# Kernel optimization log

Hardware: AMD Instinct MI355X
Metric: run time of the kernel (lower is better)

Reference implementation:

```python
import jax, jax.numpy as jnp
import numpy as np

B, S, I, H, O, E, K = 2, 2048, 4096, 1376, 4096, 8, 2
BALANCE_W = 0.01  # balance_loss_weight in llama-moe


def setup_inputs() -> dict:
    key = jax.random.key(0)
    ks = jax.random.split(key, 6)
    sc = lambda k, shape, fan: jax.random.normal(k, shape, jnp.float32) * (fan ** -0.5)
    return {
        "x": jax.random.normal(ks[0], (B, S, I), jnp.float32),
        "gate_w": sc(ks[1], (E, I), I),          # linear gate network, no bias
        "w_gate": sc(ks[2], (E, H, I), I),       # GLU gate proj per expert
        "b_gate": jnp.zeros((E, H), jnp.float32),
        "w_up": sc(ks[3], (E, H, I), I),         # GLU up proj per expert
        "b_up": jnp.zeros((E, H), jnp.float32),
        "w_down": sc(ks[4], (E, O, H), H),       # down proj per expert
        "b_down": jnp.zeros((E, O), jnp.float32),
    }


def _cv_squared(v, eps=1e-10):
    # torch: x.var() / (x.mean()**2 + eps), unbiased variance
    mean = jnp.mean(v)
    var = jnp.sum((v - mean) ** 2) / (v.shape[0] - 1)
    return var / (mean ** 2 + eps)


def reference(x, gate_w, w_gate, b_gate, w_up, b_up, w_down, b_down):
    bsz, seq, _ = x.shape
    xt = x.reshape(-1, I)                         # [T, I] tokens
    T = xt.shape[0]

    # ---- TopKBalancedNoisyGate (no-noise branch) ----
    logits = xt @ gate_w.T                        # [T, E]
    top_logits, top_idx = jax.lax.top_k(logits, K)
    top_scores = jax.nn.softmax(top_logits, axis=-1)   # softmax over top-k logits
    # dense routing matrix: zeros.scatter(1, top_idx, top_scores)
    dense = jnp.zeros((T, E), xt.dtype).at[jnp.arange(T)[:, None], top_idx].set(top_scores)
    importance = dense.sum(axis=0)                # [E]
    load = (dense > 0).astype(jnp.float32).sum(axis=0)  # [E]
    gate_loss = BALANCE_W * (_cv_squared(importance) + _cv_squared(load))

    # ---- UniversalCalculator over LinearGLUExperts ----
    # Dense-dispatch formulation: compute every expert on every token, weight by
    # the (mostly-zero) routing matrix -> identical math to gather/grouped-GEMM/scatter.
    g = jnp.einsum('ti,ehi->teh', xt, w_gate) + b_gate        # [T, E, H]
    u = jnp.einsum('ti,ehi->teh', xt, w_up) + b_up            # [T, E, H]
    inter = jax.nn.silu(g) * u                                # GLU
    # score * (W_down h + b_down) == W_down (score*h) + score*b_down
    y = jnp.einsum('teh,eoh->to', inter * dense[:, :, None], w_down) + dense @ b_down
    return y.reshape(bsz, seq, O), gate_loss
```

## Files before the change

kernel.cpp:

```cpp
#include <hip/hip_runtime.h>
#include <hip/hip_bf16.h>
#include <stdint.h>

#define TN 4096
#define DI 4096
#define DH 1376
#define DHP 1408
#define DO 4096
#define NE 8
#define NPAIR 8192

typedef unsigned short u16;
typedef __bf16 bf16x8 __attribute__((ext_vector_type(8)));
typedef float f32x4 __attribute__((ext_vector_type(4)));
typedef uint32_t u32x4 __attribute__((ext_vector_type(4)));

__device__ __forceinline__ uint32_t pack2bf(float a, float b) {
    union { float f; uint32_t u; } ua, ub;
    ua.f = a; ub.f = b;
    uint32_t lo = (ua.u + 0x7fffu + ((ua.u >> 16) & 1u)) >> 16;
    uint32_t hi = (ub.u + 0x7fffu + ((ub.u >> 16) & 1u)) >> 16;
    return lo | (hi << 16);
}
__device__ __forceinline__ u16 f2bf(float a) {
    union { float f; uint32_t u; } ua; ua.f = a;
    return (u16)((ua.u + 0x7fffu + ((ua.u >> 16) & 1u)) >> 16);
}
__device__ __forceinline__ void gload16(const void* g, void* l) {
    __builtin_amdgcn_global_load_lds(
        (const __attribute__((address_space(1))) void*)g,
        (__attribute__((address_space(3))) void*)l, 16, 0, 0);
}

__global__ __launch_bounds__(256) void k_cvt(const float* __restrict__ src,
                                             u16* __restrict__ dst, int n8)
{
    int i = blockIdx.x * 256 + threadIdx.x;
    if (i >= n8) return;
    const float4* s = (const float4*)(src + (size_t)i * 8);
    float4 a = s[0], b = s[1];
    u32x4 q = {pack2bf(a.x, a.y), pack2bf(a.z, a.w), pack2bf(b.x, b.y), pack2bf(b.z, b.w)};
    *(u32x4*)(dst + (size_t)i * 8) = q;
}

__global__ __launch_bounds__(256) void k_cvt_wd(const float* __restrict__ src,
                                                u16* __restrict__ dst)
{
    int i = blockIdx.x * 256 + threadIdx.x;
    int row = i / 176, c8 = (i % 176) * 8;
    u32x4 q = {0u, 0u, 0u, 0u};
    if (c8 < DH) {
        const float4* s = (const float4*)(src + (size_t)row * DH + c8);
        float4 a = s[0], b = s[1];
        q = (u32x4){pack2bf(a.x, a.y), pack2bf(a.z, a.w), pack2bf(b.x, b.y), pack2bf(b.z, b.w)};
    }
    *(u32x4*)(dst + (size_t)row * DHP + c8) = q;
}

__global__ __launch_bounds__(256) void k_gate(
    const float* __restrict__ x, const float* __restrict__ gw,
    u16* __restrict__ x16, int* __restrict__ tke, float* __restrict__ tks,
    int* __restrict__ cnt, float* __restrict__ imp)
{
    int t = blockIdx.x, tid = threadIdx.x;
    const float* xr = x + (size_t)t * DI;
    double acc[NE];
#pragma unroll
    for (int e = 0; e < NE; ++e) acc[e] = 0.0;
#pragma unroll
    for (int j = 0; j < 4; ++j) {
        int i4 = (j * 256 + tid) * 4;
        float4 xv = *(const float4*)(xr + i4);
        uint2 p; p.x = pack2bf(xv.x, xv.y); p.y = pack2bf(xv.z, xv.w);
        *(uint2*)(x16 + (size_t)t * DI + i4) = p;
#pragma unroll
        for (int e = 0; e < NE; ++e) {
            float4 wv = *(const float4*)(gw + (size_t)e * DI + i4);
            acc[e] = fma((double)xv.x, (double)wv.x, acc[e]);
            acc[e] = fma((double)xv.y, (double)wv.y, acc[e]);
            acc[e] = fma((double)xv.z, (double)wv.z, acc[e]);
            acc[e] = fma((double)xv.w, (double)wv.w, acc[e]);
        }
    }
#pragma unroll
    for (int o = 32; o > 0; o >>= 1)
#pragma unroll
        for (int e = 0; e < NE; ++e) acc[e] += __shfl_down(acc[e], o, 64);
    __shared__ double lred[4][NE];
    if ((tid & 63) == 0)
#pragma unroll
        for (int e = 0; e < NE; ++e) lred[tid >> 6][e] = acc[e];
    __syncthreads();
    if (tid == 0) {
        double lg[NE];
#pragma unroll
        for (int e = 0; e < NE; ++e) lg[e] = lred[0][e] + lred[1][e] + lred[2][e] + lred[3][e];
        int e1 = 0;
        for (int e = 1; e < NE; ++e) if (lg[e] > lg[e1]) e1 = e;
        int e2 = -1;
        for (int e = 0; e < NE; ++e) { if (e == e1) continue; if (e2 < 0 || lg[e] > lg[e2]) e2 = e; }
        float d = (float)(lg[e2] - lg[e1]);
        float ed = expf(d);
        float s1 = 1.0f / (1.0f + ed);
        float s2 = ed / (1.0f + ed);
        tke[2 * t] = e1; tke[2 * t + 1] = e2;
        tks[2 * t] = s1; tks[2 * t + 1] = s2;
        atomicAdd(&cnt[e1], 1); atomicAdd(&cnt[e2], 1);
        unsafeAtomicAdd(&imp[e1], s1); unsafeAtomicAdd(&imp[e2], s2);
    }
}

__global__ void k_finalize(const int* __restrict__ cnt, const float* __restrict__ imp,
                           int* __restrict__ off, float* __restrict__ loss_out)
{
    if (threadIdx.x == 0 && blockIdx.x == 0) {
        int o = 0;
        for (int e = 0; e < NE; ++e) { off[e] = o; o += cnt[e]; }
        float m1 = 0.f, m2 = 0.f;
        for (int e = 0; e < NE; ++e) { m1 += imp[e]; m2 += (float)cnt[e]; }
        m1 *= 0.125f; m2 *= 0.125f;
        float v1 = 0.f, v2 = 0.f;
        for (int e = 0; e < NE; ++e) {
            float d1 = imp[e] - m1, d2 = (float)cnt[e] - m2;
            v1 += d1 * d1; v2 += d2 * d2;
        }
        v1 /= 7.0f; v2 /= 7.0f;
        float cv1 = v1 / (m1 * m1 + 1e-10f);
        float cv2 = v2 / (m2 * m2 + 1e-10f);
        *loss_out = 0.01f * (cv1 + cv2);
    }
}

__global__ __launch_bounds__(256) void k_scatter(
    const int* __restrict__ tke, const float* __restrict__ tks,
    const int* __restrict__ off, int* __restrict__ fill,
    int* __restrict__ tok, float* __restrict__ sc)
{
    int t = blockIdx.x * 256 + threadIdx.x;
    if (t >= TN) return;
#pragma unroll
    for (int k = 0; k < 2; ++k) {
        int e = tke[2 * t + k];
        int pos = off[e] + atomicAdd(&fill[e], 1);
        tok[pos] = t; sc[pos] = tks[2 * t + k];
    }
}

__global__ __launch_bounds__(256) void k_yinit(
    const int* __restrict__ tke, const float* __restrict__ tks,
    const float* __restrict__ bd, float* __restrict__ y)
{
    int t = blockIdx.x, tid = threadIdx.x;
    int e1 = tke[2 * t], e2 = tke[2 * t + 1];
    float s1 = tks[2 * t], s2 = tks[2 * t + 1];
    const float4* b1 = (const float4*)(bd + (size_t)e1 * DO);
    const float4* b2 = (const float4*)(bd + (size_t)e2 * DO);
    float4* yr = (float4*)(y + (size_t)t * DO);
#pragma unroll
    for (int j = 0; j < 4; ++j) {
        int i = j * 256 + tid;
        float4 a = b1[i], b = b2[i], r;
        r.x = s1 * a.x + s2 * b.x; r.y = s1 * a.y + s2 * b.y;
        r.z = s1 * a.z + s2 * b.z; r.w = s1 * a.w + s2 * b.w;
        yr[i] = r;
    }
}


__global__ __launch_bounds__(256, 2) void k_stage1f(
    const u16* __restrict__ x16,
    const u16* __restrict__ wg16, const u16* __restrict__ wu16,
    const float* __restrict__ bg, const float* __restrict__ bu,
    const int* __restrict__ cnt, const int* __restrict__ off,
    const int* __restrict__ tok, const float* __restrict__ sc,
    u16* __restrict__ inter)
{
    int e = blockIdx.x & 7;
    int ce = cnt[e];
    int rows0 = (blockIdx.x >> 3) * 128;
    if (rows0 >= ce) return;
    int oe = off[e];
    int h0 = blockIdx.y * 128;
    int tid = threadIdx.x;

    __shared__ u16 As0[128 * 32]; __shared__ u16 As1[128 * 32];
    __shared__ u16 Gs0[128 * 32]; __shared__ u16 Gs1[128 * 32];
    __shared__ u16 Us0[128 * 32]; __shared__ u16 Us1[128 * 32];

    int swz = ((tid & 3) ^ ((tid >> 3) & 3)) * 8;
    const u16* ab0; const u16* ab1; const u16* gb0; const u16* gb1;
    const u16* ub0; const u16* ub1;
    {
        int rl0 = tid >> 2, rl1 = 64 + (tid >> 2);
        int rg0 = oe + min(rows0 + rl0, ce - 1);
        int rg1 = oe + min(rows0 + rl1, ce - 1);
        ab0 = x16 + (size_t)tok[rg0] * DI + swz;
        ab1 = x16 + (size_t)tok[rg1] * DI + swz;
        int hr0 = min(h0 + rl0, DH - 1), hr1 = min(h0 + rl1, DH - 1);
        gb0 = wg16 + ((size_t)e * DH + hr0) * DI + swz;
        gb1 = wg16 + ((size_t)e * DH + hr1) * DI + swz;
        ub0 = wu16 + ((size_t)e * DH + hr0) * DI + swz;
        ub1 = wu16 + ((size_t)e * DH + hr1) * DI + swz;
    }

    int wid = tid >> 6, lane = tid & 63;
    int ldsw = wid * 512;
    int wm = wid >> 1, wn = wid & 1;
    int rA = wm * 64 + (lane & 15);
    int rB = wn * 64 + (lane & 15);
    int colb = (((lane >> 4) ^ ((lane >> 1) & 3)) & 3) * 8;

    f32x4 accg[4][4], accu[4][4];
    f32x4 vz = {0.f, 0.f, 0.f, 0.f};
#pragma unroll
    for (int m = 0; m < 4; ++m)
#pragma unroll
        for (int n = 0; n < 4; ++n) { accg[m][n] = vz; accu[m][n] = vz; }

#define S1_STAGE(A_, G_, U_, K0)                                   \
    do {                                                           \
        gload16(ab0 + (K0), &A_[ldsw]);                            \
        gload16(ab1 + (K0), &A_[2048 + ldsw]);                     \
        gload16(gb0 + (K0), &G_[ldsw]);                            \
        gload16(gb1 + (K0), &G_[2048 + ldsw]);                     \
        gload16(ub0 + (K0), &U_[ldsw]);                            \
        gload16(ub1 + (K0), &U_[2048 + ldsw]);                     \
    } while (0)

#define S1_COMPUTE(A_, G_, U_)                                     \
    do {                                                           \
        bf16x8 a[4], g[4], u[4];                                   \
        _Pragma("unroll")                                          \
        for (int m = 0; m < 4; ++m)                                \
            a[m] = *(const bf16x8*)&A_[(rA + m * 16) * 32 + colb]; \
        _Pragma("unroll")                                          \
        for (int n = 0; n < 4; ++n) {                              \
            g[n] = *(const bf16x8*)&G_[(rB + n * 16) * 32 + colb]; \
            u[n] = *(const bf16x8*)&U_[(rB + n * 16) * 32 + colb]; \
        }                                                          \
        _Pragma("unroll")                                          \
        for (int m = 0; m < 4; ++m)                                \
            _Pragma("unroll")                                      \
            for (int n = 0; n < 4; ++n) {                          \
                accg[m][n] = __builtin_amdgcn_mfma_f32_16x16x32_bf16(a[m], g[n], accg[m][n], 0, 0, 0); \
                accu[m][n] = __builtin_amdgcn_mfma_f32_16x16x32_bf16(a[m], u[n], accu[m][n], 0, 0, 0); \
            }                                                      \
    } while (0)

    S1_STAGE(As0, Gs0, Us0, 0);
    __syncthreads();

    const int NT = DI / 32;
    for (int kt = 0; kt < NT; kt += 2) {
        if (kt + 1 < NT) S1_STAGE(As1, Gs1, Us1, (kt + 1) * 32);
        S1_COMPUTE(As0, Gs0, Us0);
        __syncthreads();
        if (kt + 2 < NT) S1_STAGE(As0, Gs0, Us0, (kt + 2) * 32);
        S1_COMPUTE(As1, Gs1, Us1);
        __syncthreads();
    }
#undef S1_STAGE
#undef S1_COMPUTE

    int rmax = ce - rows0;
    float bgv[4], buv[4];
    int hc[4]; bool hok[4];
#pragma unroll
    for (int n = 0; n < 4; ++n) {
        hc[n] = h0 + wn * 64 + n * 16 + (lane & 15);
        hok[n] = hc[n] < DH;
        bgv[n] = hok[n] ? bg[e * DH + hc[n]] : 0.f;
        buv[n] = hok[n] ? bu[e * DH + hc[n]] : 0.f;
    }
#pragma unroll
    for (int m = 0; m < 4; ++m) {
#pragma unroll
        for (int r = 0; r < 4; ++r) {
            int rl = wm * 64 + m * 16 + (lane >> 4) * 4 + r;
            if (rl < rmax) {
                int rg = oe + rows0 + rl;
                float s = sc[rg];
                size_t rowb = (size_t)rg * DHP;
#pragma unroll
                for (int n = 0; n < 4; ++n) {
                    float v = 0.f;
                    if (hok[n]) {
                        float gv = accg[m][n][r] + bgv[n];
                        float uv = accu[m][n][r] + buv[n];
                        float sig = 1.0f / (1.0f + __expf(-gv));
                        v = s * gv * sig * uv;
                    }
                    inter[rowb + hc[n]] = f2bf(v);
                }
            }
        }
    }
}

__global__ __launch_bounds__(256, 2) void k_stage2f(
    const u16* __restrict__ inter, const u16* __restrict__ wd16,
    const int* __restrict__ cnt, const int* __restrict__ off,
    const int* __restrict__ tok, float* __restrict__ y)
{
    int e = blockIdx.x & 7;
    int ce = cnt[e];
    int rows0 = (blockIdx.x >> 3) * 128;
    if (rows0 >= ce) return;
    int oe = off[e];
    int o0 = blockIdx.y * 128;
    int tid = threadIdx.x;

    __shared__ u16 As0[128 * 32]; __shared__ u16 As1[128 * 32];
    __shared__ u16 Bs0[128 * 32]; __shared__ u16 Bs1[128 * 32];

    int swz = ((tid & 3) ^ ((tid >> 3) & 3)) * 8;
    const u16* ab0; const u16* ab1; const u16* bb0; const u16* bb1;
    {
        int rl0 = tid >> 2, rl1 = 64 + (tid >> 2);
        int ar0 = min(oe + rows0 + rl0, NPAIR - 1);
        int ar1 = min(oe + rows0 + rl1, NPAIR - 1);
        ab0 = inter + (size_t)ar0 * DHP + swz;
        ab1 = inter + (size_t)ar1 * DHP + swz;
        bb0 = wd16 + ((size_t)e * DO + (o0 + rl0)) * DHP + swz;
        bb1 = wd16 + ((size_t)e * DO + (o0 + rl1)) * DHP + swz;
    }

    int wid = tid >> 6, lane = tid & 63;
    int ldsw = wid * 512;
    int wm = wid >> 1, wn = wid & 1;
    int rA = wm * 64 + (lane & 15);
    int rB = wn * 64 + (lane & 15);
    int colb = (((lane >> 4) ^ ((lane >> 1) & 3)) & 3) * 8;

    f32x4 acc[4][4];
    f32x4 vz = {0.f, 0.f, 0.f, 0.f};
#pragma unroll
    for (int m = 0; m < 4; ++m)
#pragma unroll
        for (int n = 0; n < 4; ++n) acc[m][n] = vz;

#define S2_STAGE(A_, B_, K0)                                       \
    do {                                                           \
        gload16(ab0 + (K0), &A_[ldsw]);                            \
        gload16(ab1 + (K0), &A_[2048 + ldsw]);                     \
        gload16(bb0 + (K0), &B_[ldsw]);                            \
        gload16(bb1 + (K0), &B_[2048 + ldsw]);                     \
    } while (0)

#define S2_COMPUTE(A_, B_)                                         \
    do {                                                           \
        bf16x8 a[4], b[4];                                         \
        _Pragma("unroll")                                          \
        for (int m = 0; m < 4; ++m)                                \
            a[m] = *(const bf16x8*)&A_[(rA + m * 16) * 32 + colb]; \
        _Pragma("unroll")                                          \
        for (int n = 0; n < 4; ++n)                                \
            b[n] = *(const bf16x8*)&B_[(rB + n * 16) * 32 + colb]; \
        _Pragma("unroll")                                          \
        for (int m = 0; m < 4; ++m)                                \
            _Pragma("unroll")                                      \
            for (int n = 0; n < 4; ++n)                            \
                acc[m][n] = __builtin_amdgcn_mfma_f32_16x16x32_bf16(a[m], b[n], acc[m][n], 0, 0, 0); \
    } while (0)

    S2_STAGE(As0, Bs0, 0);
    __syncthreads();

    const int NT = DHP / 32;
    for (int kt = 0; kt < NT; kt += 2) {
        if (kt + 1 < NT) S2_STAGE(As1, Bs1, (kt + 1) * 32);
        S2_COMPUTE(As0, Bs0);
        __syncthreads();
        if (kt + 2 < NT) S2_STAGE(As0, Bs0, (kt + 2) * 32);
        S2_COMPUTE(As1, Bs1);
        __syncthreads();
    }
#undef S2_STAGE
#undef S2_COMPUTE

    int rmax = ce - rows0;
#pragma unroll
    for (int m = 0; m < 4; ++m) {
#pragma unroll
        for (int r = 0; r < 4; ++r) {
            int rl = wm * 64 + m * 16 + (lane >> 4) * 4 + r;
            if (rl >= rmax) continue;
            int t = tok[oe + rows0 + rl];
            float* yr = y + (size_t)t * DO + o0 + wn * 64 + (lane & 15);
#pragma unroll
            for (int n = 0; n < 4; ++n)
                unsafeAtomicAdd(yr + n * 16, acc[m][n][r]);
        }
    }
}

extern "C" void kernel_launch(void* const* d_in, const int* in_sizes, int n_in,
                              void* d_out, int out_size, void* d_ws, size_t ws_size,
                              hipStream_t stream)
{
    const float* x  = (const float*)d_in[0];
    const float* gw = (const float*)d_in[1];
    const float* wg = (const float*)d_in[2];
    const float* bg = (const float*)d_in[3];
    const float* wu = (const float*)d_in[4];
    const float* bu = (const float*)d_in[5];
    const float* wd = (const float*)d_in[6];
    const float* bd = (const float*)d_in[7];
    float* y = (float*)d_out;
    float* loss = y + (size_t)TN * DO;

    uint8_t* ws = (uint8_t*)d_ws;
    u16*   x16   = (u16*)(ws + 0);
    u16*   inter = (u16*)(ws + 33554432ull);
    u16*   wg16  = (u16*)(ws + 56623104ull);
    u16*   wu16  = (u16*)(ws + 146800640ull);
    u16*   wd16  = (u16*)(ws + 236978176ull);
    int*   tok   = (int*)(ws + 329252864ull);
    float* sc    = (float*)(ws + 329285632ull);
    int*   tke   = (int*)(ws + 329318400ull);
    float* tks   = (float*)(ws + 329351168ull);
    int*   misc  = (int*)(ws + 329383936ull);
    int* cnt = misc; int* fill = misc + 8; int* off = misc + 16;
    float* imp = (float*)(misc + 24);

    hipMemsetAsync(misc, 0, 128, stream);
    k_cvt<<<22016, 256, 0, stream>>>(wg, wg16, 5636096);
    k_cvt<<<22016, 256, 0, stream>>>(wu, wu16, 5636096);
    k_cvt_wd<<<22528, 256, 0, stream>>>(wd, wd16);
    k_gate<<<TN, 256, 0, stream>>>(x, gw, x16, tke, tks, cnt, imp);
    k_finalize<<<1, 64, 0, stream>>>(cnt, imp, off, loss);
    k_scatter<<<TN / 256, 256, 0, stream>>>(tke, tks, off, fill, tok, sc);
    k_yinit<<<TN, 256, 0, stream>>>(tke, tks, bd, y);
    k_stage1f<<<dim3(256, 11), 256, 0, stream>>>(x16, wg16, wu16, bg, bu, cnt, off, tok, sc, inter);
    k_stage2f<<<dim3(256, 32), 256, 0, stream>>>(inter, wd16, cnt, off, tok, y);
}
```

Measured before the change: 801.2 us.

## Triple-buffer LDS pipeline with vmcnt waits and MFMA priority in expert GEMMs

Both grouped expert GEMM kernels move from a double-buffered loop with __syncthreads to a three-stage LDS ring. Two tiles of global->LDS loads stay in flight, and each stage waits only on its own loads through explicit s_waitcnt vmcnt counts plus raw s_barrier. Wave priority is raised around the MFMA block so compute issues ahead of the loads. This is meant to hide global load latency better, at the cost of 50% more LDS per block, which may limit occupancy. The hand-counted vmcnt values make correctness depend on the exact number of loads per stage.

```diff
diff --git a/kernel.cpp b/kernel.cpp
--- a/kernel.cpp
+++ b/kernel.cpp
@@ -31,6 +31,7 @@
         (const __attribute__((address_space(1))) void*)g,
         (__attribute__((address_space(3))) void*)l, 16, 0, 0);
 }
+#define MEMFENCE() asm volatile("" ::: "memory")
 
 __global__ __launch_bounds__(256) void k_cvt(const float* __restrict__ src,
                                              u16* __restrict__ dst, int n8)
@@ -167,7 +168,7 @@
 }
 
 
-__global__ __launch_bounds__(256, 2) void k_stage1f(
+__global__ __launch_bounds__(256, 2) void k_stage1g(
     const u16* __restrict__ x16,
     const u16* __restrict__ wg16, const u16* __restrict__ wu16,
     const float* __restrict__ bg, const float* __restrict__ bu,
@@ -183,9 +184,9 @@
     int h0 = blockIdx.y * 128;
     int tid = threadIdx.x;
 
-    __shared__ u16 As0[128 * 32]; __shared__ u16 As1[128 * 32];
-    __shared__ u16 Gs0[128 * 32]; __shared__ u16 Gs1[128 * 32];
-    __shared__ u16 Us0[128 * 32]; __shared__ u16 Us1[128 * 32];
+    __shared__ u16 As0[128 * 32]; __shared__ u16 As1[128 * 32]; __shared__ u16 As2[128 * 32];
+    __shared__ u16 Gs0[128 * 32]; __shared__ u16 Gs1[128 * 32]; __shared__ u16 Gs2[128 * 32];
+    __shared__ u16 Us0[128 * 32]; __shared__ u16 Us1[128 * 32]; __shared__ u16 Us2[128 * 32];
 
     int swz = ((tid & 3) ^ ((tid >> 3) & 3)) * 8;
     const u16* ab0; const u16* ab1; const u16* gb0; const u16* gb1;
@@ -238,6 +239,7 @@
             g[n] = *(const bf16x8*)&G_[(rB + n * 16) * 32 + colb]; \
             u[n] = *(const bf16x8*)&U_[(rB + n * 16) * 32 + colb]; \
         }                                                          \
+        __builtin_amdgcn_s_setprio(1);                             \
         _Pragma("unroll")                                          \
         for (int m = 0; m < 4; ++m)                                \
             _Pragma("unroll")                                      \
@@ -245,22 +247,43 @@
                 accg[m][n] = __builtin_amdgcn_mfma_f32_16x16x32_bf16(a[m], g[n], accg[m][n], 0, 0, 0); \
                 accu[m][n] = __builtin_amdgcn_mfma_f32_16x16x32_bf16(a[m], u[n], accu[m][n], 0, 0, 0); \
             }                                                      \
-    } while (0)
-
+        __builtin_amdgcn_s_setprio(0);                             \
+    } while (0)
+
+#define S1_PHASE(A_, G_, U_, KN)                                   \
+    do {                                                           \
+        asm volatile("s_waitcnt vmcnt(12)" ::: "memory");          \
+        __builtin_amdgcn_s_barrier();                              \
+        MEMFENCE();                                                \
+        S1_COMPUTE(A_, G_, U_);                                    \
+        __builtin_amdgcn_s_barrier();                              \
+        MEMFENCE();                                                \
+        S1_STAGE(A_, G_, U_, KN);                                  \
+    } while (0)
+
+    const int NT = DI / 32;
+    const int KL = (NT - 1) * 32;
     S1_STAGE(As0, Gs0, Us0, 0);
-    __syncthreads();
-
-    const int NT = DI / 32;
-    for (int kt = 0; kt < NT; kt += 2) {
-        if (kt + 1 < NT) S1_STAGE(As1, Gs1, Us1, (kt + 1) * 32);
-        S1_COMPUTE(As0, Gs0, Us0);
-        __syncthreads();
-        if (kt + 2 < NT) S1_STAGE(As0, Gs0, Us0, (kt + 2) * 32);
-        S1_COMPUTE(As1, Gs1, Us1);
-        __syncthreads();
-    }
+    S1_STAGE(As1, Gs1, Us1, 32);
+    S1_STAGE(As2, Gs2, Us2, 64);
+
+    for (int kt = 0; kt + 4 < NT; kt += 3) {
+        S1_PHASE(As0, Gs0, Us0, min((kt + 3) * 32, KL));
+        S1_PHASE(As1, Gs1, Us1, min((kt + 4) * 32, KL));
+        S1_PHASE(As2, Gs2, Us2, min((kt + 5) * 32, KL));
+    }
+    asm volatile("s_waitcnt vmcnt(12)" ::: "memory");
+    __builtin_amdgcn_s_barrier();
+    MEMFENCE();
+    S1_COMPUTE(As0, Gs0, Us0);
+    asm volatile("s_waitcnt vmcnt(6)" ::: "memory");
+    __builtin_amdgcn_s_barrier();
+    MEMFENCE();
+    S1_COMPUTE(As1, Gs1, Us1);
+    asm volatile("s_waitcnt vmcnt(0)" ::: "memory");
 #undef S1_STAGE
 #undef S1_COMPUTE
+#undef S1_PHASE
 
     int rmax = ce - rows0;
     float bgv[4], buv[4];
@@ -297,7 +320,7 @@
     }
 }
 
-__global__ __launch_bounds__(256, 2) void k_stage2f(
+__global__ __launch_bounds__(256, 2) void k_stage2g(
     const u16* __restrict__ inter, const u16* __restrict__ wd16,
     const int* __restrict__ cnt, const int* __restrict__ off,
     const int* __restrict__ tok, float* __restrict__ y)
@@ -310,8 +333,8 @@
     int o0 = blockIdx.y * 128;
     int tid = threadIdx.x;
 
-    __shared__ u16 As0[128 * 32]; __shared__ u16 As1[128 * 32];
-    __shared__ u16 Bs0[128 * 32]; __shared__ u16 Bs1[128 * 32];
+    __shared__ u16 As0[128 * 32]; __shared__ u16 As1[128 * 32]; __shared__ u16 As2[128 * 32];
+    __shared__ u16 Bs0[128 * 32]; __shared__ u16 Bs1[128 * 32]; __shared__ u16 Bs2[128 * 32];
 
     int swz = ((tid & 3) ^ ((tid >> 3) & 3)) * 8;
     const u16* ab0; const u16* ab1; const u16* bb0; const u16* bb1;
@@ -356,27 +379,49 @@
         _Pragma("unroll")                                          \
         for (int n = 0; n < 4; ++n)                                \
             b[n] = *(const bf16x8*)&B_[(rB + n * 16) * 32 + colb]; \
+        __builtin_amdgcn_s_setprio(1);                             \
         _Pragma("unroll")                                          \
         for (int m = 0; m < 4; ++m)                                \
             _Pragma("unroll")                                      \
             for (int n = 0; n < 4; ++n)                            \
                 acc[m][n] = __builtin_amdgcn_mfma_f32_16x16x32_bf16(a[m], b[n], acc[m][n], 0, 0, 0); \
-    } while (0)
-
+        __builtin_amdgcn_s_setprio(0);                             \
+    } while (0)
+
+#define S2_PHASE(A_, B_, KN)                                       \
+    do {                                                           \
+        asm volatile("s_waitcnt vmcnt(8)" ::: "memory");           \
+        __builtin_amdgcn_s_barrier();                              \
+        MEMFENCE();                                                \
+        S2_COMPUTE(A_, B_);                                        \
+        __builtin_amdgcn_s_barrier();                              \
+        MEMFENCE();                                                \
+        S2_STAGE(A_, B_, KN);                                      \
+    } while (0)
+
+    const int NT = DHP / 32;
+    const int KL = (NT - 1) * 32;
     S2_STAGE(As0, Bs0, 0);
-    __syncthreads();
-
-    const int NT = DHP / 32;
-    for (int kt = 0; kt < NT; kt += 2) {
-        if (kt + 1 < NT) S2_STAGE(As1, Bs1, (kt + 1) * 32);
-        S2_COMPUTE(As0, Bs0);
-        __syncthreads();
-        if (kt + 2 < NT) S2_STAGE(As0, Bs0, (kt + 2) * 32);
-        S2_COMPUTE(As1, Bs1);
-        __syncthreads();
-    }
+    S2_STAGE(As1, Bs1, 32);
+    S2_STAGE(As2, Bs2, 64);
+
+    for (int kt = 0; kt + 4 < NT; kt += 3) {
+        S2_PHASE(As0, Bs0, min((kt + 3) * 32, KL));
+        S2_PHASE(As1, Bs1, min((kt + 4) * 32, KL));
+        S2_PHASE(As2, Bs2, min((kt + 5) * 32, KL));
+    }
+    asm volatile("s_waitcnt vmcnt(8)" ::: "memory");
+    __builtin_amdgcn_s_barrier();
+    MEMFENCE();
+    S2_COMPUTE(As0, Bs0);
+    asm volatile("s_waitcnt vmcnt(4)" ::: "memory");
+    __builtin_amdgcn_s_barrier();
+    MEMFENCE();
+    S2_COMPUTE(As1, Bs1);
+    asm volatile("s_waitcnt vmcnt(0)" ::: "memory");
 #undef S2_STAGE
 #undef S2_COMPUTE
+#undef S2_PHASE
 
     int rmax = ce - rows0;
 #pragma unroll
@@ -431,6 +476,6 @@
     k_finalize<<<1, 64, 0, stream>>>(cnt, imp, off, loss);
     k_scatter<<<TN / 256, 256, 0, stream>>>(tke, tks, off, fill, tok, sc);
     k_yinit<<<TN, 256, 0, stream>>>(tke, tks, bd, y);
-    k_stage1f<<<dim3(256, 11), 256, 0, stream>>>(x16, wg16, wu16, bg, bu, cnt, off, tok, sc, inter);
-    k_stage2f<<<dim3(256, 32), 256, 0, stream>>>(inter, wd16, cnt, off, tok, y);
-}
+    k_stage1g<<<dim3(256, 11), 256, 0, stream>>>(x16, wg16, wu16, bg, bu, cnt, off, tok, sc, inter);
+    k_stage2g<<<dim3(256, 32), 256, 0, stream>>>(inter, wd16, cnt, off, tok, y);
+}
```

Result: no change. 793.4 us (-1.0%).

## Keep two K-tiles in flight with explicit vmcnt waits and MFMA priority

Applied to the files above, without the earlier changes.

Both grouped-GEMM kernels are restructured so two stages of global-to-LDS loads are always outstanding. Each stage waits only on the older batch with s_waitcnt vmcnt(N) and a raw s_barrier, where before every __syncthreads drained all loads. The MFMA block is wrapped in s_setprio(1)/s_setprio(0) so the matrix math gets issue priority over other waves. The goal is to hide global memory latency behind compute, at the cost of relying on hand-counted vmcnt values that must match the number of loads issued per stage.

```diff
diff --git a/kernel.cpp b/kernel.cpp
--- a/kernel.cpp
+++ b/kernel.cpp
@@ -31,6 +31,7 @@
         (const __attribute__((address_space(1))) void*)g,
         (__attribute__((address_space(3))) void*)l, 16, 0, 0);
 }
+#define MEMFENCE() asm volatile("" ::: "memory")
 
 __global__ __launch_bounds__(256) void k_cvt(const float* __restrict__ src,
                                              u16* __restrict__ dst, int n8)
@@ -167,7 +168,7 @@
 }
 
 
-__global__ __launch_bounds__(256, 2) void k_stage1f(
+__global__ __launch_bounds__(256, 2) void k_stage1h(
     const u16* __restrict__ x16,
     const u16* __restrict__ wg16, const u16* __restrict__ wu16,
     const float* __restrict__ bg, const float* __restrict__ bu,
@@ -238,6 +239,7 @@
             g[n] = *(const bf16x8*)&G_[(rB + n * 16) * 32 + colb]; \
             u[n] = *(const bf16x8*)&U_[(rB + n * 16) * 32 + colb]; \
         }                                                          \
+        __builtin_amdgcn_s_setprio(1);                             \
         _Pragma("unroll")                                          \
         for (int m = 0; m < 4; ++m)                                \
             _Pragma("unroll")                                      \
@@ -245,20 +247,37 @@
                 accg[m][n] = __builtin_amdgcn_mfma_f32_16x16x32_bf16(a[m], g[n], accg[m][n], 0, 0, 0); \
                 accu[m][n] = __builtin_amdgcn_mfma_f32_16x16x32_bf16(a[m], u[n], accu[m][n], 0, 0, 0); \
             }                                                      \
+        __builtin_amdgcn_s_setprio(0);                             \
     } while (0)
 
+    const int NT = DI / 32;
     S1_STAGE(As0, Gs0, Us0, 0);
-    __syncthreads();
-
-    const int NT = DI / 32;
-    for (int kt = 0; kt < NT; kt += 2) {
-        if (kt + 1 < NT) S1_STAGE(As1, Gs1, Us1, (kt + 1) * 32);
+    S1_STAGE(As1, Gs1, Us1, 32);
+
+    for (int kt = 0; kt < NT - 2; kt += 2) {
+        asm volatile("s_waitcnt vmcnt(6)" ::: "memory");
+        __builtin_amdgcn_s_barrier();
+        MEMFENCE();
         S1_COMPUTE(As0, Gs0, Us0);
-        __syncthreads();
-        if (kt + 2 < NT) S1_STAGE(As0, Gs0, Us0, (kt + 2) * 32);
+        __builtin_amdgcn_s_barrier();
+        MEMFENCE();
+        S1_STAGE(As0, Gs0, Us0, (kt + 2) * 32);
+        asm volatile("s_waitcnt vmcnt(6)" ::: "memory");
+        __builtin_amdgcn_s_barrier();
+        MEMFENCE();
         S1_COMPUTE(As1, Gs1, Us1);
-        __syncthreads();
-    }
+        __builtin_amdgcn_s_barrier();
+        MEMFENCE();
+        S1_STAGE(As1, Gs1, Us1, (kt + 3) * 32);
+    }
+    asm volatile("s_waitcnt vmcnt(6)" ::: "memory");
+    __builtin_amdgcn_s_barrier();
+    MEMFENCE();
+    S1_COMPUTE(As0, Gs0, Us0);
+    asm volatile("s_waitcnt vmcnt(0)" ::: "memory");
+    __builtin_amdgcn_s_barrier();
+    MEMFENCE();
+    S1_COMPUTE(As1, Gs1, Us1);
 #undef S1_STAGE
 #undef S1_COMPUTE
 
@@ -297,7 +316,7 @@
     }
 }
 
-__global__ __launch_bounds__(256, 2) void k_stage2f(
+__global__ __launch_bounds__(256, 2) void k_stage2h(
     const u16* __restrict__ inter, const u16* __restrict__ wd16,
     const int* __restrict__ cnt, const int* __restrict__ off,
     const int* __restrict__ tok, float* __restrict__ y)
@@ -356,25 +375,43 @@
         _Pragma("unroll")                                          \
         for (int n = 0; n < 4; ++n)                                \
             b[n] = *(const bf16x8*)&B_[(rB + n * 16) * 32 + colb]; \
+        __builtin_amdgcn_s_setprio(1);                             \
         _Pragma("unroll")                                          \
         for (int m = 0; m < 4; ++m)                                \
             _Pragma("unroll")                                      \
             for (int n = 0; n < 4; ++n)                            \
                 acc[m][n] = __builtin_amdgcn_mfma_f32_16x16x32_bf16(a[m], b[n], acc[m][n], 0, 0, 0); \
+        __builtin_amdgcn_s_setprio(0);                             \
     } while (0)
 
+    const int NT = DHP / 32;
     S2_STAGE(As0, Bs0, 0);
-    __syncthreads();
-
-    const int NT = DHP / 32;
-    for (int kt = 0; kt < NT; kt += 2) {
-        if (kt + 1 < NT) S2_STAGE(As1, Bs1, (kt + 1) * 32);
+    S2_STAGE(As1, Bs1, 32);
+
+    for (int kt = 0; kt < NT - 2; kt += 2) {
+        asm volatile("s_waitcnt vmcnt(4)" ::: "memory");
+        __builtin_amdgcn_s_barrier();
+        MEMFENCE();
         S2_COMPUTE(As0, Bs0);
-        __syncthreads();
-        if (kt + 2 < NT) S2_STAGE(As0, Bs0, (kt + 2) * 32);
+        __builtin_amdgcn_s_barrier();
+        MEMFENCE();
+        S2_STAGE(As0, Bs0, (kt + 2) * 32);
+        asm volatile("s_waitcnt vmcnt(4)" ::: "memory");
+        __builtin_amdgcn_s_barrier();
+        MEMFENCE();
         S2_COMPUTE(As1, Bs1);
-        __syncthreads();
-    }
+        __builtin_amdgcn_s_barrier();
+        MEMFENCE();
+        S2_STAGE(As1, Bs1, (kt + 3) * 32);
+    }
+    asm volatile("s_waitcnt vmcnt(4)" ::: "memory");
+    __builtin_amdgcn_s_barrier();
+    MEMFENCE();
+    S2_COMPUTE(As0, Bs0);
+    asm volatile("s_waitcnt vmcnt(0)" ::: "memory");
+    __builtin_amdgcn_s_barrier();
+    MEMFENCE();
+    S2_COMPUTE(As1, Bs1);
 #undef S2_STAGE
 #undef S2_COMPUTE
 
@@ -431,6 +468,6 @@
     k_finalize<<<1, 64, 0, stream>>>(cnt, imp, off, loss);
     k_scatter<<<TN / 256, 256, 0, stream>>>(tke, tks, off, fill, tok, sc);
     k_yinit<<<TN, 256, 0, stream>>>(tke, tks, bd, y);
-    k_stage1f<<<dim3(256, 11), 256, 0, stream>>>(x16, wg16, wu16, bg, bu, cnt, off, tok, sc, inter);
-    k_stage2f<<<dim3(256, 32), 256, 0, stream>>>(inter, wd16, cnt, off, tok, y);
-}
+    k_stage1h<<<dim3(256, 11), 256, 0, stream>>>(x16, wg16, wu16, bg, bu, cnt, off, tok, sc, inter);
+    k_stage2h<<<dim3(256, 32), 256, 0, stream>>>(inter, wd16, cnt, off, tok, y);
+}
```

After: 800.0 us. No clear change (-0.2%).

## Rewrite grouped GEMM kernels with 512-thread 256-row tiles and ping-pong schedule

Applied to the files above, without the earlier changes.

Both expert GEMM stages move to 512-thread blocks with 256-row token tiles, K-step 64, and an 8-way XOR-swizzled LDS layout. The main loop interleaves LDS reads, async global-to-LDS loads and MFMA bursts between explicit barriers, with s_setprio raised around the MFMA bursts. Stage 2 also widens its output tile to 256 columns, so each wave holds 8x4 accumulators. This is meant to raise data reuse per LDS byte and overlap loads with compute. In exchange it uses more LDS and registers per block, and for small experts more of each 256-row tile is padding.

```diff
diff --git a/kernel.cpp b/kernel.cpp
--- a/kernel.cpp
+++ b/kernel.cpp
@@ -31,6 +31,11 @@
         (const __attribute__((address_space(1))) void*)g,
         (__attribute__((address_space(3))) void*)l, 16, 0, 0);
 }
+#define MEMFENCE() asm volatile("" ::: "memory")
+#define VMCNT0()   asm volatile("s_waitcnt vmcnt(0)" ::: "memory")
+#define BAR()      do { MEMFENCE(); __builtin_amdgcn_s_barrier(); MEMFENCE(); } while (0)
+#define LGKM()     do { asm volatile("s_waitcnt lgkmcnt(0)" ::: "memory"); \
+                        __builtin_amdgcn_sched_barrier(0); } while (0)
 
 __global__ __launch_bounds__(256) void k_cvt(const float* __restrict__ src,
                                              u16* __restrict__ dst, int n8)
@@ -167,7 +172,7 @@
 }
 
 
-__global__ __launch_bounds__(256, 2) void k_stage1f(
+__global__ __launch_bounds__(512, 2) void k_s1_8p(
     const u16* __restrict__ x16,
     const u16* __restrict__ wg16, const u16* __restrict__ wu16,
     const float* __restrict__ bg, const float* __restrict__ bu,
@@ -177,38 +182,38 @@
 {
     int e = blockIdx.x & 7;
     int ce = cnt[e];
-    int rows0 = (blockIdx.x >> 3) * 128;
+    int rows0 = (blockIdx.x >> 3) * 256;
     if (rows0 >= ce) return;
     int oe = off[e];
     int h0 = blockIdx.y * 128;
     int tid = threadIdx.x;
 
-    __shared__ u16 As0[128 * 32]; __shared__ u16 As1[128 * 32];
-    __shared__ u16 Gs0[128 * 32]; __shared__ u16 Gs1[128 * 32];
-    __shared__ u16 Us0[128 * 32]; __shared__ u16 Us1[128 * 32];
-
-    int swz = ((tid & 3) ^ ((tid >> 3) & 3)) * 8;
-    const u16* ab0; const u16* ab1; const u16* gb0; const u16* gb1;
-    const u16* ub0; const u16* ub1;
-    {
-        int rl0 = tid >> 2, rl1 = 64 + (tid >> 2);
-        int rg0 = oe + min(rows0 + rl0, ce - 1);
-        int rg1 = oe + min(rows0 + rl1, ce - 1);
-        ab0 = x16 + (size_t)tok[rg0] * DI + swz;
-        ab1 = x16 + (size_t)tok[rg1] * DI + swz;
-        int hr0 = min(h0 + rl0, DH - 1), hr1 = min(h0 + rl1, DH - 1);
-        gb0 = wg16 + ((size_t)e * DH + hr0) * DI + swz;
-        gb1 = wg16 + ((size_t)e * DH + hr1) * DI + swz;
-        ub0 = wu16 + ((size_t)e * DH + hr0) * DI + swz;
-        ub1 = wu16 + ((size_t)e * DH + hr1) * DI + swz;
+    __shared__ u16 Aa[256 * 64]; __shared__ u16 Ab[256 * 64];
+    __shared__ u16 Ga[128 * 64]; __shared__ u16 Gb[128 * 64];
+    __shared__ u16 Ua[128 * 64]; __shared__ u16 Ub[128 * 64];
+
+    int swz = ((tid & 7) ^ ((tid >> 3) & 7)) * 8;
+    int rr = tid >> 3;
+    const u16* ap[4]; const u16* gp[2]; const u16* up[2];
+#pragma unroll
+    for (int i = 0; i < 4; ++i) {
+        int rg = oe + min(rows0 + i * 64 + rr, ce - 1);
+        ap[i] = x16 + (size_t)tok[rg] * DI + swz;
+    }
+#pragma unroll
+    for (int j = 0; j < 2; ++j) {
+        int hr = min(h0 + j * 64 + rr, DH - 1);
+        gp[j] = wg16 + ((size_t)e * DH + hr) * DI + swz;
+        up[j] = wu16 + ((size_t)e * DH + hr) * DI + swz;
     }
 
     int wid = tid >> 6, lane = tid & 63;
-    int ldsw = wid * 512;
     int wm = wid >> 1, wn = wid & 1;
-    int rA = wm * 64 + (lane & 15);
-    int rB = wn * 64 + (lane & 15);
-    int colb = (((lane >> 4) ^ ((lane >> 1) & 3)) & 3) * 8;
+    int l15 = lane & 15, q = lane >> 4;
+    int ph0 = ((q ^ (lane & 7)) & 7) * 8;
+    int ph1 = (((4 + q) ^ (lane & 7)) & 7) * 8;
+    int rAb = (wm * 64 + l15) * 64;
+    int rBb = (wn * 64 + l15) * 64;
 
     f32x4 accg[4][4], accu[4][4];
     f32x4 vz = {0.f, 0.f, 0.f, 0.f};
@@ -217,57 +222,71 @@
 #pragma unroll
         for (int n = 0; n < 4; ++n) { accg[m][n] = vz; accu[m][n] = vz; }
 
-#define S1_STAGE(A_, G_, U_, K0)                                   \
-    do {                                                           \
-        gload16(ab0 + (K0), &A_[ldsw]);                            \
-        gload16(ab1 + (K0), &A_[2048 + ldsw]);                     \
-        gload16(gb0 + (K0), &G_[ldsw]);                            \
-        gload16(gb1 + (K0), &G_[2048 + ldsw]);                     \
-        gload16(ub0 + (K0), &U_[ldsw]);                            \
-        gload16(ub1 + (K0), &U_[2048 + ldsw]);                     \
-    } while (0)
-
-#define S1_COMPUTE(A_, G_, U_)                                     \
-    do {                                                           \
-        bf16x8 a[4], g[4], u[4];                                   \
-        _Pragma("unroll")                                          \
-        for (int m = 0; m < 4; ++m)                                \
-            a[m] = *(const bf16x8*)&A_[(rA + m * 16) * 32 + colb]; \
-        _Pragma("unroll")                                          \
-        for (int n = 0; n < 4; ++n) {                              \
-            g[n] = *(const bf16x8*)&G_[(rB + n * 16) * 32 + colb]; \
-            u[n] = *(const bf16x8*)&U_[(rB + n * 16) * 32 + colb]; \
-        }                                                          \
-        _Pragma("unroll")                                          \
-        for (int m = 0; m < 4; ++m)                                \
-            _Pragma("unroll")                                      \
-            for (int n = 0; n < 4; ++n) {                          \
-                accg[m][n] = __builtin_amdgcn_mfma_f32_16x16x32_bf16(a[m], g[n], accg[m][n], 0, 0, 0); \
-                accu[m][n] = __builtin_amdgcn_mfma_f32_16x16x32_bf16(a[m], u[n], accu[m][n], 0, 0, 0); \
-            }                                                      \
-    } while (0)
-
-    S1_STAGE(As0, Gs0, Us0, 0);
-    __syncthreads();
-
-    const int NT = DI / 32;
-    for (int kt = 0; kt < NT; kt += 2) {
-        if (kt + 1 < NT) S1_STAGE(As1, Gs1, Us1, (kt + 1) * 32);
-        S1_COMPUTE(As0, Gs0, Us0);
-        __syncthreads();
-        if (kt + 2 < NT) S1_STAGE(As0, Gs0, Us0, (kt + 2) * 32);
-        S1_COMPUTE(As1, Gs1, Us1);
-        __syncthreads();
-    }
-#undef S1_STAGE
-#undef S1_COMPUTE
+#define RD_A(DST, T_, PH) \
+    _Pragma("unroll") for (int m = 0; m < 4; ++m) \
+        DST[m] = *(const bf16x8*)&T_[rAb + m * 1024 + (PH)];
+#define RD_B(DST, T_, PH) \
+    _Pragma("unroll") for (int n = 0; n < 4; ++n) \
+        DST[n] = *(const bf16x8*)&T_[rBb + n * 1024 + (PH)];
+#define MM16(ACC, AV, BV) \
+    do { __builtin_amdgcn_s_setprio(1); \
+    _Pragma("unroll") for (int m = 0; m < 4; ++m) \
+    _Pragma("unroll") for (int n = 0; n < 4; ++n) \
+        ACC[m][n] = __builtin_amdgcn_mfma_f32_16x16x32_bf16(AV[m], BV[n], ACC[m][n], 0, 0, 0); \
+    __builtin_amdgcn_s_setprio(0); } while (0)
+#define STA(T_, K0) \
+    _Pragma("unroll") for (int i = 0; i < 4; ++i) \
+        gload16(ap[i] + (K0), &T_[i * 4096 + wid * 512]);
+#define STGU(G_, U_, K0) \
+    _Pragma("unroll") for (int j = 0; j < 2; ++j) { \
+        gload16(gp[j] + (K0), &G_[j * 4096 + wid * 512]); \
+        gload16(up[j] + (K0), &U_[j * 4096 + wid * 512]); }
+
+#define S1_TILE(A_, G_, U_, An, Gn, Un, K0, DOST)   \
+  do {                                              \
+    bf16x8 av[4], bv[4];                            \
+    RD_A(av, A_, ph0); RD_B(bv, G_, ph0);           \
+    if (DOST) { STA(An, K0); }                      \
+    BAR(); LGKM();                                  \
+    MM16(accg, av, bv);                             \
+    BAR();                                          \
+    RD_B(bv, U_, ph0);                              \
+    if (DOST) { STGU(Gn, Un, K0); }                 \
+    BAR(); LGKM();                                  \
+    MM16(accu, av, bv);                             \
+    BAR();                                          \
+    RD_A(av, A_, ph1); RD_B(bv, G_, ph1);           \
+    BAR(); LGKM();                                  \
+    MM16(accg, av, bv);                             \
+    BAR();                                          \
+    RD_B(bv, U_, ph1);                              \
+    BAR(); LGKM();                                  \
+    MM16(accu, av, bv);                             \
+    VMCNT0();                                       \
+    BAR();                                          \
+  } while (0)
+
+    STA(Aa, 0); STGU(Ga, Ua, 0);
+    VMCNT0();
+    BAR();
+
+    const int NT = DI / 64;
+    for (int t = 0; t < NT; t += 2) {
+        S1_TILE(Aa, Ga, Ua, Ab, Gb, Ub, (t + 1) * 64, (t + 1) < NT);
+        S1_TILE(Ab, Gb, Ub, Aa, Ga, Ua, (t + 2) * 64, (t + 2) < NT);
+    }
+#undef S1_TILE
+#undef STA
+#undef STGU
+#undef RD_A
+#undef RD_B
 
     int rmax = ce - rows0;
     float bgv[4], buv[4];
     int hc[4]; bool hok[4];
 #pragma unroll
     for (int n = 0; n < 4; ++n) {
-        hc[n] = h0 + wn * 64 + n * 16 + (lane & 15);
+        hc[n] = h0 + wn * 64 + n * 16 + l15;
         hok[n] = hc[n] < DH;
         bgv[n] = hok[n] ? bg[e * DH + hc[n]] : 0.f;
         buv[n] = hok[n] ? bu[e * DH + hc[n]] : 0.f;
@@ -276,7 +295,7 @@
     for (int m = 0; m < 4; ++m) {
 #pragma unroll
         for (int r = 0; r < 4; ++r) {
-            int rl = wm * 64 + m * 16 + (lane >> 4) * 4 + r;
+            int rl = wm * 64 + m * 16 + q * 4 + r;
             if (rl < rmax) {
                 int rg = oe + rows0 + rl;
                 float s = sc[rg];
@@ -297,96 +316,110 @@
     }
 }
 
-__global__ __launch_bounds__(256, 2) void k_stage2f(
+__global__ __launch_bounds__(512, 2) void k_s2_8p(
     const u16* __restrict__ inter, const u16* __restrict__ wd16,
     const int* __restrict__ cnt, const int* __restrict__ off,
     const int* __restrict__ tok, float* __restrict__ y)
 {
     int e = blockIdx.x & 7;
     int ce = cnt[e];
-    int rows0 = (blockIdx.x >> 3) * 128;
+    int rows0 = (blockIdx.x >> 3) * 256;
     if (rows0 >= ce) return;
     int oe = off[e];
-    int o0 = blockIdx.y * 128;
+    int o0 = blockIdx.y * 256;
     int tid = threadIdx.x;
 
-    __shared__ u16 As0[128 * 32]; __shared__ u16 As1[128 * 32];
-    __shared__ u16 Bs0[128 * 32]; __shared__ u16 Bs1[128 * 32];
-
-    int swz = ((tid & 3) ^ ((tid >> 3) & 3)) * 8;
-    const u16* ab0; const u16* ab1; const u16* bb0; const u16* bb1;
-    {
-        int rl0 = tid >> 2, rl1 = 64 + (tid >> 2);
-        int ar0 = min(oe + rows0 + rl0, NPAIR - 1);
-        int ar1 = min(oe + rows0 + rl1, NPAIR - 1);
-        ab0 = inter + (size_t)ar0 * DHP + swz;
-        ab1 = inter + (size_t)ar1 * DHP + swz;
-        bb0 = wd16 + ((size_t)e * DO + (o0 + rl0)) * DHP + swz;
-        bb1 = wd16 + ((size_t)e * DO + (o0 + rl1)) * DHP + swz;
+    __shared__ u16 Aa[256 * 64]; __shared__ u16 Ab[256 * 64];
+    __shared__ u16 Ba[256 * 64]; __shared__ u16 Bb[256 * 64];
+
+    int swz = ((tid & 7) ^ ((tid >> 3) & 7)) * 8;
+    int rr = tid >> 3;
+    const u16* ap[4]; const u16* bp[4];
+#pragma unroll
+    for (int i = 0; i < 4; ++i) {
+        int ar = min(oe + rows0 + i * 64 + rr, NPAIR - 1);
+        ap[i] = inter + (size_t)ar * DHP + swz;
+        bp[i] = wd16 + ((size_t)e * DO + (o0 + i * 64 + rr)) * DHP + swz;
     }
 
     int wid = tid >> 6, lane = tid & 63;
-    int ldsw = wid * 512;
-    int wm = wid >> 1, wn = wid & 1;
-    int rA = wm * 64 + (lane & 15);
-    int rB = wn * 64 + (lane & 15);
-    int colb = (((lane >> 4) ^ ((lane >> 1) & 3)) & 3) * 8;
-
-    f32x4 acc[4][4];
+    int wm = wid >> 2, wn = wid & 3;
+    int l15 = lane & 15, q = lane >> 4;
+    int ph0 = ((q ^ (lane & 7)) & 7) * 8;
+    int ph1 = (((4 + q) ^ (lane & 7)) & 7) * 8;
+    int rAb = (wm * 128 + l15) * 64;
+    int rBb = (wn * 64 + l15) * 64;
+
+    f32x4 acc[8][4];
     f32x4 vz = {0.f, 0.f, 0.f, 0.f};
 #pragma unroll
-    for (int m = 0; m < 4; ++m)
+    for (int m = 0; m < 8; ++m)
 #pragma unroll
         for (int n = 0; n < 4; ++n) acc[m][n] = vz;
 
-#define S2_STAGE(A_, B_, K0)                                       \
-    do {                                                           \
-        gload16(ab0 + (K0), &A_[ldsw]);                            \
-        gload16(ab1 + (K0), &A_[2048 + ldsw]);                     \
-        gload16(bb0 + (K0), &B_[ldsw]);                            \
-        gload16(bb1 + (K0), &B_[2048 + ldsw]);                     \
-    } while (0)
-
-#define S2_COMPUTE(A_, B_)                                         \
-    do {                                                           \
-        bf16x8 a[4], b[4];                                         \
-        _Pragma("unroll")                                          \
-        for (int m = 0; m < 4; ++m)                                \
-            a[m] = *(const bf16x8*)&A_[(rA + m * 16) * 32 + colb]; \
-        _Pragma("unroll")                                          \
-        for (int n = 0; n < 4; ++n)                                \
-            b[n] = *(const bf16x8*)&B_[(rB + n * 16) * 32 + colb]; \
-        _Pragma("unroll")                                          \
-        for (int m = 0; m < 4; ++m)                                \
-            _Pragma("unroll")                                      \
-            for (int n = 0; n < 4; ++n)                            \
-                acc[m][n] = __builtin_amdgcn_mfma_f32_16x16x32_bf16(a[m], b[n], acc[m][n], 0, 0, 0); \
-    } while (0)
-
-    S2_STAGE(As0, Bs0, 0);
-    __syncthreads();
-
-    const int NT = DHP / 32;
-    for (int kt = 0; kt < NT; kt += 2) {
-        if (kt + 1 < NT) S2_STAGE(As1, Bs1, (kt + 1) * 32);
-        S2_COMPUTE(As0, Bs0);
-        __syncthreads();
-        if (kt + 2 < NT) S2_STAGE(As0, Bs0, (kt + 2) * 32);
-        S2_COMPUTE(As1, Bs1);
-        __syncthreads();
-    }
-#undef S2_STAGE
-#undef S2_COMPUTE
+#define RD_A2(DST, T_, PH, MB) \
+    _Pragma("unroll") for (int m = 0; m < 4; ++m) \
+        DST[m] = *(const bf16x8*)&T_[rAb + ((MB) + m) * 1024 + (PH)];
+#define RD_B2(DST, T_, PH) \
+    _Pragma("unroll") for (int n = 0; n < 4; ++n) \
+        DST[n] = *(const bf16x8*)&T_[rBb + n * 1024 + (PH)];
+#define MM16_2(MB, AV, BV) \
+    do { __builtin_amdgcn_s_setprio(1); \
+    _Pragma("unroll") for (int m = 0; m < 4; ++m) \
+    _Pragma("unroll") for (int n = 0; n < 4; ++n) \
+        acc[(MB) + m][n] = __builtin_amdgcn_mfma_f32_16x16x32_bf16(AV[m], BV[n], acc[(MB) + m][n], 0, 0, 0); \
+    __builtin_amdgcn_s_setprio(0); } while (0)
+#define ST4(P_, T_, K0) \
+    _Pragma("unroll") for (int i = 0; i < 4; ++i) \
+        gload16(P_[i] + (K0), &T_[i * 4096 + wid * 512]);
+
+#define S2_TILE(A_, B_, An, Bn, K0, DOST)           \
+  do {                                              \
+    bf16x8 av[4], bv[4];                            \
+    RD_A2(av, A_, ph0, 0); RD_B2(bv, B_, ph0);      \
+    if (DOST) { ST4(ap, An, K0); }                  \
+    BAR(); LGKM();                                  \
+    MM16_2(0, av, bv);                              \
+    BAR();                                          \
+    RD_A2(av, A_, ph0, 4);                          \
+    if (DOST) { ST4(bp, Bn, K0); }                  \
+    BAR(); LGKM();                                  \
+    MM16_2(4, av, bv);                              \
+    BAR();                                          \
+    RD_A2(av, A_, ph1, 0); RD_B2(bv, B_, ph1);      \
+    BAR(); LGKM();                                  \
+    MM16_2(0, av, bv);                              \
+    BAR();                                          \
+    RD_A2(av, A_, ph1, 4);                          \
+    BAR(); LGKM();                                  \
+    MM16_2(4, av, bv);                              \
+    VMCNT0();                                       \
+    BAR();                                          \
+  } while (0)
+
+    ST4(ap, Aa, 0); ST4(bp, Ba, 0);
+    VMCNT0();
+    BAR();
+
+    const int NT = DHP / 64;
+    for (int t = 0; t < NT; t += 2) {
+        S2_TILE(Aa, Ba, Ab, Bb, (t + 1) * 64, (t + 1) < NT);
+        S2_TILE(Ab, Bb, Aa, Ba, (t + 2) * 64, (t + 2) < NT);
+    }
+#undef S2_TILE
+#undef ST4
+#undef RD_A2
+#undef RD_B2
 
     int rmax = ce - rows0;
 #pragma unroll
-    for (int m = 0; m < 4; ++m) {
+    for (int m = 0; m < 8; ++m) {
 #pragma unroll
         for (int r = 0; r < 4; ++r) {
-            int rl = wm * 64 + m * 16 + (lane >> 4) * 4 + r;
+            int rl = wm * 128 + m * 16 + q * 4 + r;
             if (rl >= rmax) continue;
             int t = tok[oe + rows0 + rl];
-            float* yr = y + (size_t)t * DO + o0 + wn * 64 + (lane & 15);
+            float* yr = y + (size_t)t * DO + o0 + wn * 64 + l15;
 #pragma unroll
             for (int n = 0; n < 4; ++n)
                 unsafeAtomicAdd(yr + n * 16, acc[m][n][r]);
@@ -431,6 +464,6 @@
     k_finalize<<<1, 64, 0, stream>>>(cnt, imp, off, loss);
     k_scatter<<<TN / 256, 256, 0, stream>>>(tke, tks, off, fill, tok, sc);
     k_yinit<<<TN, 256, 0, stream>>>(tke, tks, bd, y);
-    k_stage1f<<<dim3(256, 11), 256, 0, stream>>>(x16, wg16, wu16, bg, bu, cnt, off, tok, sc, inter);
-    k_stage2f<<<dim3(256, 32), 256, 0, stream>>>(inter, wd16, cnt, off, tok, y);
-}
+    k_s1_8p<<<dim3(128, 11), 512, 0, stream>>>(x16, wg16, wu16, bg, bu, cnt, off, tok, sc, inter);
+    k_s2_8p<<<dim3(128, 16), 512, 0, stream>>>(inter, wd16, cnt, off, tok, y);
+}
```

Result: slower. 962.4 us (+20.1%).
